# Kernel tuning notes

Hardware: AMD Instinct MI355X
Metric: run time of the kernel (lower is better)

The kernel has to match this reference:

```python
import jax, jax.numpy as jnp
import numpy as np

D_MODEL = 1024
NUM_HEADS = 16
HEAD_DIM = D_MODEL // NUM_HEADS
B, S = 2, 2048


def setup_inputs() -> dict:
    key = jax.random.key(0)
    ks = jax.random.split(key, 10)
    sc = 1.0 / np.sqrt(D_MODEL)
    return {
        "x": jax.random.normal(ks[0], (B, S, D_MODEL), jnp.float32),
        "y": jax.random.normal(ks[1], (B, S, D_MODEL), jnp.float32),
        "Wkv": jax.random.normal(ks[2], (D_MODEL, 2 * D_MODEL), jnp.float32) * sc,
        "bkv": jax.random.normal(ks[3], (2 * D_MODEL,), jnp.float32) * 0.01,
        "Wq": jax.random.normal(ks[4], (D_MODEL, D_MODEL), jnp.float32) * sc,
        "bq": jax.random.normal(ks[5], (D_MODEL,), jnp.float32) * 0.01,
        "Wo": jax.random.normal(ks[6], (D_MODEL, D_MODEL), jnp.float32) * sc,
        "bo": jax.random.normal(ks[7], (D_MODEL,), jnp.float32) * 0.01,
    }


def reference(x, y, Wkv, bkv, Wq, bq, Wo, bo):
    b, s, d = x.shape
    # projections: kv from x (keys/values come from encoder side), q from y
    kv = x @ Wkv + bkv                      # [B, S, 2*d_model]
    q = y @ Wq + bq                         # [B, S, d_model]
    kv = kv.reshape(b, s, NUM_HEADS, 2 * HEAD_DIM).transpose(0, 2, 1, 3)  # [B,H,S,2*hd]
    q = q.reshape(b, s, NUM_HEADS, HEAD_DIM).transpose(0, 2, 1, 3)        # [B,H,S,hd]
    k, v = jnp.split(kv, 2, axis=-1)        # each [B,H,S,hd]
    scaled = jnp.einsum("bhqd,bhkd->bhqk", q, k) / np.sqrt(HEAD_DIM)      # [B,H,S,S]
    attention = jax.nn.softmax(scaled, axis=-1)
    values = jnp.einsum("bhqk,bhkd->bhqd", attention, v)                  # [B,H,S,hd]
    values = values.transpose(0, 2, 1, 3).reshape(b, s, d)                # [B,S,d_model]
    return values @ Wo + bo
```

## Files before the change

### kernel.cpp

```cpp
#include <hip/hip_runtime.h>
#include <hip/hip_bf16.h>

typedef __attribute__((ext_vector_type(8))) short short8;
typedef __attribute__((ext_vector_type(4))) short short4v;
typedef __attribute__((ext_vector_type(4))) float f32x4;

#define B_  2
#define S_  2048
#define H_  16
#define HD_ 64
#define D_  1024
#define QSCALE 0.18033688f

__device__ __forceinline__ short f2bs(float f) {
  union { float f; unsigned u; } c; c.f = f;
  unsigned u = c.u;
  u += 0x7fffu + ((u >> 16) & 1u);
  return (short)(u >> 16);
}

__device__ __forceinline__ unsigned pack_bf16(float a, float b) {
  __hip_bfloat162 h = __float22bfloat162_rn(float2{a, b});
  return *reinterpret_cast<unsigned*>(&h);
}

__device__ __forceinline__ float fexp2(float x) {
#if __has_builtin(__builtin_amdgcn_exp2f)
  return __builtin_amdgcn_exp2f(x);
#else
  return exp2f(x);
#endif
}

__device__ __forceinline__ float frcp(float x) {
#if __has_builtin(__builtin_amdgcn_rcpf)
  return __builtin_amdgcn_rcpf(x);
#else
  return 1.0f / x;
#endif
}

#define GL2LDS(gp, lp) __builtin_amdgcn_global_load_lds( \
    (const __attribute__((address_space(1))) unsigned int*)(gp), \
    (__attribute__((address_space(3))) unsigned int*)(lp), 16, 0, 0)

__global__ __launch_bounds__(256)
void prep_kernel(const float* __restrict__ x, const float* __restrict__ y,
                 short* __restrict__ xb, short* __restrict__ yb,
                 const float* __restrict__ Wkv, short* __restrict__ Wkvt,
                 const float* __restrict__ Wq, short* __restrict__ Wqt,
                 const float* __restrict__ Wo, short* __restrict__ Wot) {
  __shared__ float tile[64][65];
  int bx = blockIdx.x;
  if (bx < 8192) {
    int i = bx * 256 + threadIdx.x;
    const float4* src; short4v* dst; int j;
    if (i < (1 << 20)) { src = (const float4*)x; dst = (short4v*)xb; j = i; }
    else               { src = (const float4*)y; dst = (short4v*)yb; j = i - (1 << 20); }
    float4 f = src[j];
    short4v o;
    o.x = f2bs(f.x); o.y = f2bs(f.y); o.z = f2bs(f.z); o.w = f2bs(f.w);
    dst[j] = o;
    return;
  }
  bx -= 8192;
  const float* in; short* out; int C, c0, r0;
  if (bx < 512)      { in = Wkv; out = Wkvt; C = 2048; c0 = (bx & 31) * 64; r0 = (bx >> 5) * 64; }
  else if (bx < 768) { bx -= 512; in = Wq; out = Wqt; C = 1024; c0 = (bx & 15) * 64; r0 = (bx >> 4) * 64; }
  else               { bx -= 768; in = Wo; out = Wot; C = 1024; c0 = (bx & 15) * 64; r0 = (bx >> 4) * 64; }
  const int tx = threadIdx.x & 63, ty = threadIdx.x >> 6;
#pragma unroll
  for (int i = 0; i < 16; ++i) {
    int r = ty + i * 4;
    tile[r][tx] = in[(size_t)(r0 + r) * C + c0 + tx];
  }
  __syncthreads();
#pragma unroll
  for (int i = 0; i < 16; ++i) {
    int r = ty + i * 4;
    out[(size_t)(c0 + r) * 1024 + r0 + tx] = f2bs(tile[tx][r]);
  }
}

template <int MODE>
__device__ __forceinline__ void gemm_body(const short* __restrict__ A, const short* __restrict__ Bt,
                                          const float* __restrict__ bias,
                                          void* __restrict__ out0, void* __restrict__ out1,
                                          int m0, int n0, int K, short* smem) {
  short* As_ = smem;
  short* Bs_ = smem + 8192;
  const int tid = threadIdx.x;
  const int w = tid >> 6, lane = tid & 63;
  const int q15 = lane & 15, quad = lane >> 4;
  const int wm = (w >> 1) * 64, wn = (w & 1) * 64;

  f32x4 acc[4][4];
#pragma unroll
  for (int i = 0; i < 4; ++i)
#pragma unroll
    for (int j = 0; j < 4; ++j) acc[i][j] = f32x4{0.f, 0.f, 0.f, 0.f};

  const int srow = w * 16 + (lane >> 2);
  const int gch  = (lane & 3) ^ ((lane >> 3) & 3);
  const short* Ag = A + (size_t)(m0 + srow) * K + gch * 8;
  const short* Bg = Bt + (size_t)(n0 + srow) * K + gch * 8;
  const int lof = srow * 32 + (lane & 3) * 8;

  GL2LDS(Ag,                  As_ + lof);
  GL2LDS(Ag + (size_t)64 * K, As_ + lof + 2048);
  GL2LDS(Bg,                  Bs_ + lof);
  GL2LDS(Bg + (size_t)64 * K, Bs_ + lof + 2048);

  const int NT = K >> 5;
  for (int kt = 0; kt < NT; ++kt) {
    __syncthreads();
    const short* Ac = As_ + (kt & 1) * 4096;
    const short* Bc = Bs_ + (kt & 1) * 4096;
    if (kt + 1 < NT) {
      const short* a2 = Ag + (size_t)(kt + 1) * 32;
      const short* b2 = Bg + (size_t)(kt + 1) * 32;
      short* ad = As_ + ((kt & 1) ^ 1) * 4096 + lof;
      short* bd = Bs_ + ((kt & 1) ^ 1) * 4096 + lof;
      GL2LDS(a2,                  ad);
      GL2LDS(a2 + (size_t)64 * K, ad + 2048);
      GL2LDS(b2,                  bd);
      GL2LDS(b2 + (size_t)64 * K, bd + 2048);
    }
    short8 af[4], bf[4];
#pragma unroll
    for (int mi = 0; mi < 4; ++mi) {
      int rr = wm + mi * 16 + q15;
      af[mi] = *(const short8*)(Ac + rr * 32 + ((quad ^ ((rr >> 1) & 3)) * 8));
    }
#pragma unroll
    for (int ni = 0; ni < 4; ++ni) {
      int rr = wn + ni * 16 + q15;
      bf[ni] = *(const short8*)(Bc + rr * 32 + ((quad ^ ((rr >> 1) & 3)) * 8));
    }
#pragma unroll
    for (int mi = 0; mi < 4; ++mi)
#pragma unroll
      for (int ni = 0; ni < 4; ++ni)
        acc[mi][ni] = __builtin_amdgcn_mfma_f32_16x16x32_bf16(af[mi], bf[ni], acc[mi][ni], 0, 0, 0);
  }
  __syncthreads();

  if constexpr (MODE == 0) {
#pragma unroll
    for (int mi = 0; mi < 4; ++mi)
#pragma unroll
      for (int ni = 0; ni < 4; ++ni) {
        const int n = n0 + wn + ni * 16 + q15;
        const float bn = bias[n];
#pragma unroll
        for (int r = 0; r < 4; ++r) {
          const int m = m0 + wm + mi * 16 + quad * 4 + r;
          int b = m >> 11, s = m & 2047, hh = n >> 6, d = n & 63;
          ((short*)out0)[((size_t)((b * H_ + hh) * S_ + s) << 6) + d] = f2bs((acc[mi][ni][r] + bn) * QSCALE);
        }
      }
  } else {
    const int hh = n0 >> 7;
    const int bb = m0 >> 11;
    const size_t bh = (size_t)(bb * H_ + hh);
    const int s0 = m0 & 2047;
    if ((w & 1) == 0) {
#pragma unroll
      for (int mi = 0; mi < 4; ++mi)
#pragma unroll
        for (int ni = 0; ni < 4; ++ni) {
          const float bn = bias[n0 + ni * 16 + q15];
#pragma unroll
          for (int r = 0; r < 4; ++r) {
            const int s = s0 + wm + mi * 16 + quad * 4 + r;
            ((short*)out0)[((bh * S_ + s) << 6) + ni * 16 + q15] = f2bs(acc[mi][ni][r] + bn);
          }
        }
    } else {
      short* VT = smem;
#pragma unroll
      for (int mi = 0; mi < 4; ++mi)
#pragma unroll
        for (int ni = 0; ni < 4; ++ni) {
          const int d = ni * 16 + q15;
          const float bn = bias[n0 + 64 + ni * 16 + q15];
#pragma unroll
          for (int t = 0; t < 2; ++t) {
            const int chunk = (wm >> 1) + mi * 8 + quad * 2 + t;
            unsigned pk = pack_bf16(acc[mi][ni][2 * t] + bn, acc[mi][ni][2 * t + 1] + bn);
            *reinterpret_cast<unsigned*>(VT + d * 128 + ((chunk ^ (d & 15)) * 2)) = pk;
          }
        }
    }
    __syncthreads();
    {
      short* VT = smem;
      const int d = tid >> 2, t4 = tid & 3;
      unsigned vals[16];
#pragma unroll
      for (int c = 0; c < 16; ++c) {
        int chunk = t4 * 16 + c;
        vals[c] = *reinterpret_cast<unsigned*>(VT + d * 128 + ((chunk ^ (d & 15)) * 2));
      }
      uint4* dst = (uint4*)((short*)out1 + ((bh * HD_ + d) << 11) + s0 + t4 * 32);
      dst[0] = uint4{vals[0], vals[1], vals[2], vals[3]};
      dst[1] = uint4{vals[4], vals[5], vals[6], vals[7]};
      dst[2] = uint4{vals[8], vals[9], vals[10], vals[11]};
      dst[3] = uint4{vals[12], vals[13], vals[14], vals[15]};
    }
  }
}

__global__ __launch_bounds__(256)
void proj_kernel(const short* __restrict__ xb, const short* __restrict__ Wkvt,
                 const float* __restrict__ bkv, short* __restrict__ Kb, short* __restrict__ Vtb,
                 const short* __restrict__ yb, const short* __restrict__ Wqt,
                 const float* __restrict__ bq, short* __restrict__ Qb) {
  __shared__ __align__(16) short smem[16384];
  int bx = blockIdx.x;
  bx = (bx & 7) * 96 + (bx >> 3);
  if (bx < 512)
    gemm_body<1>(xb, Wkvt, bkv, Kb, Vtb, (bx >> 4) * 128, (bx & 15) * 128, 1024, smem);
  else {
    bx -= 512;
    gemm_body<0>(yb, Wqt, bq, Qb, nullptr, (bx >> 3) * 128, (bx & 7) * 128, 1024, smem);
  }
}

__global__ __launch_bounds__(256)
void gemm_o_kernel(const short* __restrict__ A, const short* __restrict__ Bt,
                   const float* __restrict__ bias, float* __restrict__ out) {
  __shared__ __align__(16) short lds[16384];
  const int tid = threadIdx.x;
  const int w = tid >> 6, lane = tid & 63;
  const int q15 = lane & 15, quad = lane >> 4;
  const int m0 = blockIdx.y * 64, n0 = blockIdx.x * 64;
  const int wm = (w >> 1) * 32, wn = (w & 1) * 32;
  const int xw = q15 & 7;

  f32x4 acc[2][2];
#pragma unroll
  for (int i = 0; i < 2; ++i)
#pragma unroll
    for (int j = 0; j < 2; ++j) acc[i][j] = f32x4{0.f, 0.f, 0.f, 0.f};

  const int srow = w * 8 + (lane >> 3);
  const int gch  = (lane & 7) ^ (srow & 7);
  const int loff = w * 512 + lane * 8;
  const short* Ag = A + (size_t)(m0 + srow) * 1024 + gch * 8;
  const short* Bg = Bt + (size_t)(n0 + srow) * 1024 + gch * 8;

  GL2LDS(Ag,             lds + loff);
  GL2LDS(Ag + 32 * 1024, lds + loff + 2048);
  GL2LDS(Bg,             lds + 8192 + loff);
  GL2LDS(Bg + 32 * 1024, lds + 8192 + loff + 2048);

  for (int kt = 0; kt < 16; ++kt) {
    __syncthreads();
    const short* Ac = lds + ((kt & 1) ? 4096 : 0);
    const short* Bc = lds + 8192 + ((kt & 1) ? 4096 : 0);
    if (kt < 15) {
      const short* a2 = Ag + (kt + 1) * 64;
      const short* b2 = Bg + (kt + 1) * 64;
      short* ad = lds + ((kt & 1) ? 0 : 4096) + loff;
      short* bd = lds + 8192 + ((kt & 1) ? 0 : 4096) + loff;
      GL2LDS(a2,             ad);
      GL2LDS(a2 + 32 * 1024, ad + 2048);
      GL2LDS(b2,             bd);
      GL2LDS(b2 + 32 * 1024, bd + 2048);
    }
    short8 af[2][2], bf[2][2];
#pragma unroll
    for (int mi = 0; mi < 2; ++mi)
#pragma unroll
      for (int kk = 0; kk < 2; ++kk)
        af[mi][kk] = *(const short8*)(Ac + (wm + mi * 16 + q15) * 64 + (((kk * 4 + quad) ^ xw) * 8));
#pragma unroll
    for (int ni = 0; ni < 2; ++ni)
#pragma unroll
      for (int kk = 0; kk < 2; ++kk)
        bf[ni][kk] = *(const short8*)(Bc + (wn + ni * 16 + q15) * 64 + (((kk * 4 + quad) ^ xw) * 8));
#pragma unroll
    for (int mi = 0; mi < 2; ++mi)
#pragma unroll
      for (int ni = 0; ni < 2; ++ni)
#pragma unroll
        for (int kk = 0; kk < 2; ++kk)
          acc[mi][ni] = __builtin_amdgcn_mfma_f32_16x16x32_bf16(af[mi][kk], bf[ni][kk], acc[mi][ni], 0, 0, 0);
  }

#pragma unroll
  for (int mi = 0; mi < 2; ++mi)
#pragma unroll
    for (int ni = 0; ni < 2; ++ni) {
      const int n = n0 + wn + ni * 16 + q15;
      const float bn = bias[n];
#pragma unroll
      for (int r = 0; r < 4; ++r) {
        const int m = m0 + wm + mi * 16 + quad * 4 + r;
        out[(size_t)m * 1024 + n] = acc[mi][ni][r] + bn;
      }
    }
}

__global__ __launch_bounds__(512, 2)
void attn_kernel(const short* __restrict__ Q, const short* __restrict__ K,
                 const short* __restrict__ Vt, short* __restrict__ Out) {
  __shared__ __align__(16) short lds[32768];
  short* QP = lds + 16384;
  const int tid = threadIdx.x;
  const int w = tid >> 6, lane = tid & 63;
  const int q15 = lane & 15, quad = lane >> 4;
  const int xw = q15 & 7;
  const int bx = blockIdx.x;
  const int xcd = bx & 7, slot = bx >> 3;
  const int pp = xcd * 4 + (slot >> 3);
  const int qt = slot & 7;
  const int h = pp & 15, b = pp >> 4;
  const size_t bh = (size_t)(b * H_ + h);
  const short* Qg = Q + bh * (S_ * HD_) + qt * (256 * HD_);
  const short* Kg = K + bh * (S_ * HD_);
  const short* Vg = Vt + bh * (HD_ * S_);

  const int srow = w * 8 + (lane >> 3);
  const int gch  = (lane & 7) ^ (srow & 7);
  const int loff = w * 512 + lane * 8;

  {
    const short* qg = Qg + srow * 64 + gch * 8;
#pragma unroll
    for (int t = 0; t < 4; ++t) GL2LDS(qg + t * 4096, QP + loff + t * 4096);
  }
  const short* kg = Kg + srow * 64 + gch * 8;
  const short* vg = Vg + (size_t)srow * S_ + gch * 8;
  GL2LDS(kg, lds + loff);
  GL2LDS(vg, lds + 8192 + loff);
  __syncthreads();

  short8 aq[2][2];
#pragma unroll
  for (int st = 0; st < 2; ++st)
#pragma unroll
    for (int kk = 0; kk < 2; ++kk)
      aq[st][kk] = *(const short8*)(QP + (w * 32 + st * 16 + q15) * 64 + (((kk * 4 + quad) ^ xw) * 8));
  short* Pb[2] = { QP + w * 2048, QP + w * 2048 + 1024 };

  f32x4 oacc[2][4];
#pragma unroll
  for (int st = 0; st < 2; ++st)
#pragma unroll
    for (int ni = 0; ni < 4; ++ni) oacc[st][ni] = f32x4{0.f, 0.f, 0.f, 0.f};
  float lsum[2] = {0.f, 0.f};
  const f32x4 zz = {0.f, 0.f, 0.f, 0.f};

  for (int kt = 0; kt < 32; ++kt) {
    __syncthreads();
    const short* Kc = lds + ((kt & 1) ? 4096 : 0);
    const short* Vc = lds + 8192 + ((kt & 1) ? 4096 : 0);
    if (kt < 31) {
      const short* k2 = kg + (kt + 1) * 4096;
      const short* v2 = vg + (kt + 1) * 64;
      GL2LDS(k2, lds + ((kt & 1) ? 0 : 4096) + loff);
      GL2LDS(v2, lds + 8192 + ((kt & 1) ? 0 : 4096) + loff);
    }

    f32x4 sacc[2][4];
#pragma unroll
    for (int mi = 0; mi < 4; ++mi) {
      const short* kr = Kc + (mi * 16 + q15) * 64;
      short8 a0 = *(const short8*)(kr + ((quad ^ xw) * 8));
      short8 a1 = *(const short8*)(kr + (((quad + 4) ^ xw) * 8));
#pragma unroll
      for (int st = 0; st < 2; ++st) {
        f32x4 t = __builtin_amdgcn_mfma_f32_16x16x32_bf16(a0, aq[st][0], zz, 0, 0, 0);
        sacc[st][mi] = __builtin_amdgcn_mfma_f32_16x16x32_bf16(a1, aq[st][1], t, 0, 0, 0);
      }
    }

#pragma unroll
    for (int st = 0; st < 2; ++st)
#pragma unroll
      for (int mi = 0; mi < 4; ++mi) {
        float p0 = fexp2(sacc[st][mi][0]), p1 = fexp2(sacc[st][mi][1]);
        float p2 = fexp2(sacc[st][mi][2]), p3 = fexp2(sacc[st][mi][3]);
        lsum[st] += (p0 + p1) + (p2 + p3);
        uint2 pk;
        pk.x = pack_bf16(p0, p1);
        pk.y = pack_bf16(p2, p3);
        *reinterpret_cast<uint2*>(Pb[st] + q15 * 64 +
                                  (((mi * 2 + (quad >> 1)) ^ xw) * 8) + (quad & 1) * 4) = pk;
      }

    short8 ap[2][2];
#pragma unroll
    for (int st = 0; st < 2; ++st)
#pragma unroll
      for (int kk = 0; kk < 2; ++kk)
        ap[st][kk] = *(const short8*)(Pb[st] + q15 * 64 + (((kk * 4 + quad) ^ xw) * 8));
#pragma unroll
    for (int ni = 0; ni < 4; ++ni) {
      const short* vr = Vc + (ni * 16 + q15) * 64;
#pragma unroll
      for (int kk = 0; kk < 2; ++kk) {
        short8 bv = *(const short8*)(vr + (((kk * 4 + quad) ^ xw) * 8));
#pragma unroll
        for (int st = 0; st < 2; ++st)
          oacc[st][ni] = __builtin_amdgcn_mfma_f32_16x16x32_bf16(ap[st][kk], bv, oacc[st][ni], 0, 0, 0);
      }
    }
  }

#pragma unroll
  for (int st = 0; st < 2; ++st) {
    float l = lsum[st];
    l += __shfl_xor(l, 16);
    l += __shfl_xor(l, 32);
    float inv[4];
#pragma unroll
    for (int r = 0; r < 4; ++r) inv[r] = frcp(__shfl(l, quad * 4 + r, 64));
#pragma unroll
    for (int ni = 0; ni < 4; ++ni) {
      const int col = h * HD_ + ni * 16 + q15;
#pragma unroll
      for (int r = 0; r < 4; ++r) {
        const int m = b * S_ + qt * 256 + w * 32 + st * 16 + quad * 4 + r;
        Out[(size_t)m * D_ + col] = f2bs(oacc[st][ni][r] * inv[r]);
      }
    }
  }
}

extern "C" void kernel_launch(void* const* d_in, const int* in_sizes, int n_in,
                              void* d_out, int out_size, void* d_ws, size_t ws_size,
                              hipStream_t stream) {
  const float* x   = (const float*)d_in[0];
  const float* y   = (const float*)d_in[1];
  const float* Wkv = (const float*)d_in[2];
  const float* bkv = (const float*)d_in[3];
  const float* Wq  = (const float*)d_in[4];
  const float* bq  = (const float*)d_in[5];
  const float* Wo  = (const float*)d_in[6];
  const float* bo  = (const float*)d_in[7];
  float* out = (float*)d_out;

  short* xb   = (short*)d_ws;
  short* yb   = xb + (4 << 20);
  short* Wkvt = yb + (4 << 20);
  short* Wqt  = Wkvt + (2 << 20);
  short* Wot  = Wqt + (1 << 20);
  short* Kb   = Wot + (1 << 20);
  short* Vtb  = Kb + (4 << 20);
  short* Qb   = Vtb + (4 << 20);
  short* AOb  = Qb + (4 << 20);

  prep_kernel<<<9216, 256, 0, stream>>>(x, y, xb, yb, Wkv, Wkvt, Wq, Wqt, Wo, Wot);
  proj_kernel<<<768, 256, 0, stream>>>(xb, Wkvt, bkv, Kb, Vtb, yb, Wqt, bq, Qb);
  attn_kernel<<<256, 512, 0, stream>>>(Qb, Kb, Vtb, AOb);
  gemm_o_kernel<<<dim3(16, 64), 256, 0, stream>>>(AOb, Wot, bo, out);
}
```

Baseline: 204.6 us.

## Switch attention to 32x32x16 MFMA and keep P in registers

The attention inner loop moves from 16x16x32 MFMAs to 32x32x16 MFMAs. The score accumulator layout is reused directly as the A operand for the PV product, so the bf16 P tile no longer round-trips through LDS. To make that register reuse valid, the V-transpose store in the projection kernel permutes the key order within each chunk. s_setprio is raised around the MFMA phases to favour matrix issue. This cuts LDS writes and reads per tile but ties correctness to the matching permutation in the projection epilogue, and it raises accumulator register pressure.

```diff
diff --git a/kernel.cpp b/kernel.cpp
--- a/kernel.cpp
+++ b/kernel.cpp
@@ -4,6 +4,7 @@
 typedef __attribute__((ext_vector_type(8))) short short8;
 typedef __attribute__((ext_vector_type(4))) short short4v;
 typedef __attribute__((ext_vector_type(4))) float f32x4;
+typedef __attribute__((ext_vector_type(16))) float f32x16;
 
 #define B_  2
 #define S_  2048
@@ -203,10 +204,10 @@
         vals[c] = *reinterpret_cast<unsigned*>(VT + d * 128 + ((chunk ^ (d & 15)) * 2));
       }
       uint4* dst = (uint4*)((short*)out1 + ((bh * HD_ + d) << 11) + s0 + t4 * 32);
-      dst[0] = uint4{vals[0], vals[1], vals[2], vals[3]};
-      dst[1] = uint4{vals[4], vals[5], vals[6], vals[7]};
-      dst[2] = uint4{vals[8], vals[9], vals[10], vals[11]};
-      dst[3] = uint4{vals[12], vals[13], vals[14], vals[15]};
+      dst[0] = uint4{vals[0], vals[1], vals[4],  vals[5]};
+      dst[1] = uint4{vals[2], vals[3], vals[6],  vals[7]};
+      dst[2] = uint4{vals[8], vals[9], vals[12], vals[13]};
+      dst[3] = uint4{vals[10], vals[11], vals[14], vals[15]};
     }
   }
 }
@@ -310,8 +311,8 @@
   short* QP = lds + 16384;
   const int tid = threadIdx.x;
   const int w = tid >> 6, lane = tid & 63;
-  const int q15 = lane & 15, quad = lane >> 4;
-  const int xw = q15 & 7;
+  const int l31 = lane & 31, h5 = lane >> 5;
+  const int rsw = l31 & 7;
   const int bx = blockIdx.x;
   const int xcd = bx & 7, slot = bx >> 3;
   const int pp = xcd * 4 + (slot >> 3);
@@ -337,21 +338,18 @@
   GL2LDS(vg, lds + 8192 + loff);
   __syncthreads();
 
-  short8 aq[2][2];
-#pragma unroll
-  for (int st = 0; st < 2; ++st)
-#pragma unroll
-    for (int kk = 0; kk < 2; ++kk)
-      aq[st][kk] = *(const short8*)(QP + (w * 32 + st * 16 + q15) * 64 + (((kk * 4 + quad) ^ xw) * 8));
-  short* Pb[2] = { QP + w * 2048, QP + w * 2048 + 1024 };
-
-  f32x4 oacc[2][4];
-#pragma unroll
-  for (int st = 0; st < 2; ++st)
-#pragma unroll
-    for (int ni = 0; ni < 4; ++ni) oacc[st][ni] = f32x4{0.f, 0.f, 0.f, 0.f};
-  float lsum[2] = {0.f, 0.f};
-  const f32x4 zz = {0.f, 0.f, 0.f, 0.f};
+  short8 aq[4];
+#pragma unroll
+  for (int kk = 0; kk < 4; ++kk)
+    aq[kk] = *(const short8*)(QP + (w * 32 + l31) * 64 + (((kk * 2 + h5) ^ rsw) * 8));
+
+  f32x16 oacc[2];
+#pragma unroll
+  for (int i = 0; i < 16; ++i) { oacc[0][i] = 0.f; oacc[1][i] = 0.f; }
+  float lsum = 0.f;
+  f32x16 z16;
+#pragma unroll
+  for (int i = 0; i < 16; ++i) z16[i] = 0.f;
 
   for (int kt = 0; kt < 32; ++kt) {
     __syncthreads();
@@ -364,68 +362,70 @@
       GL2LDS(v2, lds + 8192 + ((kt & 1) ? 0 : 4096) + loff);
     }
 
-    f32x4 sacc[2][4];
-#pragma unroll
-    for (int mi = 0; mi < 4; ++mi) {
-      const short* kr = Kc + (mi * 16 + q15) * 64;
-      short8 a0 = *(const short8*)(kr + ((quad ^ xw) * 8));
-      short8 a1 = *(const short8*)(kr + (((quad + 4) ^ xw) * 8));
-#pragma unroll
-      for (int st = 0; st < 2; ++st) {
-        f32x4 t = __builtin_amdgcn_mfma_f32_16x16x32_bf16(a0, aq[st][0], zz, 0, 0, 0);
-        sacc[st][mi] = __builtin_amdgcn_mfma_f32_16x16x32_bf16(a1, aq[st][1], t, 0, 0, 0);
-      }
-    }
-
-#pragma unroll
-    for (int st = 0; st < 2; ++st)
-#pragma unroll
-      for (int mi = 0; mi < 4; ++mi) {
-        float p0 = fexp2(sacc[st][mi][0]), p1 = fexp2(sacc[st][mi][1]);
-        float p2 = fexp2(sacc[st][mi][2]), p3 = fexp2(sacc[st][mi][3]);
-        lsum[st] += (p0 + p1) + (p2 + p3);
-        uint2 pk;
-        pk.x = pack_bf16(p0, p1);
-        pk.y = pack_bf16(p2, p3);
-        *reinterpret_cast<uint2*>(Pb[st] + q15 * 64 +
-                                  (((mi * 2 + (quad >> 1)) ^ xw) * 8) + (quad & 1) * 4) = pk;
-      }
-
-    short8 ap[2][2];
-#pragma unroll
-    for (int st = 0; st < 2; ++st)
-#pragma unroll
-      for (int kk = 0; kk < 2; ++kk)
-        ap[st][kk] = *(const short8*)(Pb[st] + q15 * 64 + (((kk * 4 + quad) ^ xw) * 8));
-#pragma unroll
-    for (int ni = 0; ni < 4; ++ni) {
-      const short* vr = Vc + (ni * 16 + q15) * 64;
-#pragma unroll
-      for (int kk = 0; kk < 2; ++kk) {
-        short8 bv = *(const short8*)(vr + (((kk * 4 + quad) ^ xw) * 8));
-#pragma unroll
-        for (int st = 0; st < 2; ++st)
-          oacc[st][ni] = __builtin_amdgcn_mfma_f32_16x16x32_bf16(ap[st][kk], bv, oacc[st][ni], 0, 0, 0);
-      }
-    }
-  }
-
-#pragma unroll
-  for (int st = 0; st < 2; ++st) {
-    float l = lsum[st];
-    l += __shfl_xor(l, 16);
-    l += __shfl_xor(l, 32);
-    float inv[4];
-#pragma unroll
-    for (int r = 0; r < 4; ++r) inv[r] = frcp(__shfl(l, quad * 4 + r, 64));
-#pragma unroll
-    for (int ni = 0; ni < 4; ++ni) {
-      const int col = h * HD_ + ni * 16 + q15;
-#pragma unroll
-      for (int r = 0; r < 4; ++r) {
-        const int m = b * S_ + qt * 256 + w * 32 + st * 16 + quad * 4 + r;
-        Out[(size_t)m * D_ + col] = f2bs(oacc[st][ni][r] * inv[r]);
-      }
+    f32x16 sacc[2];
+    __builtin_amdgcn_s_setprio(1);
+#pragma unroll
+    for (int sb = 0; sb < 2; ++sb) {
+      const short* kr = Kc + (sb * 32 + l31) * 64;
+      short8 k0 = *(const short8*)(kr + (((0 + h5) ^ rsw) * 8));
+      short8 k1 = *(const short8*)(kr + (((2 + h5) ^ rsw) * 8));
+      short8 k2 = *(const short8*)(kr + (((4 + h5) ^ rsw) * 8));
+      short8 k3 = *(const short8*)(kr + (((6 + h5) ^ rsw) * 8));
+      f32x16 s = __builtin_amdgcn_mfma_f32_32x32x16_bf16(k0, aq[0], z16, 0, 0, 0);
+      s = __builtin_amdgcn_mfma_f32_32x32x16_bf16(k1, aq[1], s, 0, 0, 0);
+      s = __builtin_amdgcn_mfma_f32_32x32x16_bf16(k2, aq[2], s, 0, 0, 0);
+      s = __builtin_amdgcn_mfma_f32_32x32x16_bf16(k3, aq[3], s, 0, 0, 0);
+      sacc[sb] = s;
+    }
+    __builtin_amdgcn_s_setprio(0);
+
+    short8 ap[4];
+#pragma unroll
+    for (int sb = 0; sb < 2; ++sb) {
+      float e[16];
+#pragma unroll
+      for (int i = 0; i < 16; ++i) e[i] = fexp2(sacc[sb][i]);
+      lsum += (((e[0] + e[1]) + (e[2] + e[3])) + ((e[4] + e[5]) + (e[6] + e[7])))
+            + (((e[8] + e[9]) + (e[10] + e[11])) + ((e[12] + e[13]) + (e[14] + e[15])));
+      union { unsigned u[4]; short8 s8; } lo, hi;
+      lo.u[0] = pack_bf16(e[0], e[1]);   lo.u[1] = pack_bf16(e[2], e[3]);
+      lo.u[2] = pack_bf16(e[4], e[5]);   lo.u[3] = pack_bf16(e[6], e[7]);
+      hi.u[0] = pack_bf16(e[8], e[9]);   hi.u[1] = pack_bf16(e[10], e[11]);
+      hi.u[2] = pack_bf16(e[12], e[13]); hi.u[3] = pack_bf16(e[14], e[15]);
+      ap[sb * 2 + 0] = lo.s8;
+      ap[sb * 2 + 1] = hi.s8;
+    }
+
+    __builtin_amdgcn_s_setprio(1);
+#pragma unroll
+    for (int db = 0; db < 2; ++db) {
+      const short* vr = Vc + (db * 32 + l31) * 64;
+      short8 v0 = *(const short8*)(vr + (((0 + h5) ^ rsw) * 8));
+      short8 v1 = *(const short8*)(vr + (((2 + h5) ^ rsw) * 8));
+      short8 v2 = *(const short8*)(vr + (((4 + h5) ^ rsw) * 8));
+      short8 v3 = *(const short8*)(vr + (((6 + h5) ^ rsw) * 8));
+      f32x16 o = oacc[db];
+      o = __builtin_amdgcn_mfma_f32_32x32x16_bf16(ap[0], v0, o, 0, 0, 0);
+      o = __builtin_amdgcn_mfma_f32_32x32x16_bf16(ap[1], v1, o, 0, 0, 0);
+      o = __builtin_amdgcn_mfma_f32_32x32x16_bf16(ap[2], v2, o, 0, 0, 0);
+      o = __builtin_amdgcn_mfma_f32_32x32x16_bf16(ap[3], v3, o, 0, 0, 0);
+      oacc[db] = o;
+    }
+    __builtin_amdgcn_s_setprio(0);
+  }
+
+  float lt = lsum + __shfl_xor(lsum, 32);
+  float inv[16];
+#pragma unroll
+  for (int r = 0; r < 16; ++r)
+    inv[r] = frcp(__shfl(lt, (r & 3) + 8 * (r >> 2) + 4 * h5, 64));
+#pragma unroll
+  for (int db = 0; db < 2; ++db) {
+    const int col = h * HD_ + db * 32 + l31;
+#pragma unroll
+    for (int r = 0; r < 16; ++r) {
+      const int m = b * S_ + qt * 256 + w * 32 + (r & 3) + 8 * (r >> 2) + 4 * h5;
+      Out[(size_t)m * D_ + col] = f2bs(oacc[db][r] * inv[r]);
     }
   }
 }
```

New measurement: 204.3 us. Within noise of the previous version (-0.2%).
